# Kernel optimization log

Hardware: AMD Instinct MI355X
Metric: run time of the kernel (lower is better)

Reference implementation:

```python
import jax, jax.numpy as jnp
import numpy as np


def setup_inputs() -> dict:
    key = jax.random.key(0)
    k1, k2, k3 = jax.random.split(key, 3)
    B, F, D = 8192, 4096, 1024
    x = jax.random.normal(k1, (B, D), dtype=jnp.float32)
    mu = jax.random.normal(k2, (F, D), dtype=jnp.float32)
    # keep scales strictly positive and well-conditioned
    scale_diag = jax.random.uniform(k3, (F, D), dtype=jnp.float32, minval=0.5, maxval=1.5)
    return {"x": x, "mu": mu, "scale_diag": scale_diag}


def reference(x, mu, scale_diag):
    # Unnormalized diag-Gaussian log prob for every (batch, feature) pair:
    #   out[b, f] = sum_d -0.5 * ((x[b,d] - mu[f,d]) / scale[f,d])^2
    # Expanded to GEMM form (quadratic expansion):
    #   -0.5 * ( x^2 @ inv2.T  -  2 * x @ (mu*inv2).T  +  sum_d mu^2*inv2 )
    inv2 = 1.0 / (scale_diag * scale_diag)            # [F, D]
    xx = jnp.matmul(x * x, inv2.T)                    # [B, F]
    xm = jnp.matmul(x, (mu * inv2).T)                 # [B, F]
    mm = jnp.sum(mu * mu * inv2, axis=-1)             # [F]
    return -0.5 * (xx - 2.0 * xm + mm[None, :])       # [B, F]
```

## Files before the change

kernel.cpp:

```cpp
#include <hip/hip_runtime.h>
#include <hip/hip_bf16.h>
#include <cstdint>

#define B_SZ 8192
#define F_SZ 4096
#define D_SZ 1024
#define K_SZ 2048

typedef __bf16 bf16x8 __attribute__((ext_vector_type(8)));
typedef float f32x4 __attribute__((ext_vector_type(4)));
typedef float fvec4 __attribute__((ext_vector_type(4)));
typedef unsigned short u16x4 __attribute__((ext_vector_type(4)));

__device__ __forceinline__ unsigned short f2bf(float f) {
    union { float f; unsigned u; } c; c.f = f;
    unsigned r = c.u + 0x7fff + ((c.u >> 16) & 1);
    return (unsigned short)(r >> 16);
}

__device__ __forceinline__ void async16(const void* g, void* l) {
    __builtin_amdgcn_global_load_lds(
        (__attribute__((address_space(1))) void*)g,
        (__attribute__((address_space(3))) void*)l, 16, 0, 0);
}

__global__ __launch_bounds__(256) void prep(const float* __restrict__ x,
                                            const float* __restrict__ mu,
                                            const float* __restrict__ sd,
                                            unsigned short* __restrict__ A,
                                            unsigned short* __restrict__ W,
                                            float* __restrict__ nmm) {
    const int tid = threadIdx.x;
    const int d = tid * 4;
    if (blockIdx.x < B_SZ) {
        const int b = blockIdx.x;
        fvec4 v = __builtin_nontemporal_load(
            (const fvec4*)(x + (size_t)b * D_SZ + d));
        u16x4 xx, xs;
        xx.x = f2bf(v.x * v.x); xx.y = f2bf(v.y * v.y);
        xx.z = f2bf(v.z * v.z); xx.w = f2bf(v.w * v.w);
        xs.x = f2bf(v.x); xs.y = f2bf(v.y); xs.z = f2bf(v.z); xs.w = f2bf(v.w);
        size_t base = (size_t)b * K_SZ;
        *(u16x4*)(A + base + d) = xx;
        *(u16x4*)(A + base + 1024 + d) = xs;
    } else {
        const int f = blockIdx.x - B_SZ;
        size_t off = (size_t)f * D_SZ + d;
        fvec4 m = __builtin_nontemporal_load((const fvec4*)(mu + off));
        fvec4 s = __builtin_nontemporal_load((const fvec4*)(sd + off));
        float i0 = 1.0f / (s.x * s.x), i1 = 1.0f / (s.y * s.y);
        float i2 = 1.0f / (s.z * s.z), i3 = 1.0f / (s.w * s.w);
        u16x4 wi, wm;
        wi.x = f2bf(i0); wi.y = f2bf(i1); wi.z = f2bf(i2); wi.w = f2bf(i3);
        wm.x = f2bf(-2.0f * m.x * i0); wm.y = f2bf(-2.0f * m.y * i1);
        wm.z = f2bf(-2.0f * m.z * i2); wm.w = f2bf(-2.0f * m.w * i3);
        size_t wb = (size_t)f * K_SZ + d;
        *(u16x4*)(W + wb) = wi;
        *(u16x4*)(W + wb + 1024) = wm;
        float mm = m.x * m.x * i0 + m.y * m.y * i1 + m.z * m.z * i2 + m.w * m.w * i3;
        #pragma unroll
        for (int o = 32; o > 0; o >>= 1) mm += __shfl_down(mm, o, 64);
        __shared__ float red[4];
        if ((tid & 63) == 0) red[tid >> 6] = mm;
        __syncthreads();
        if (tid == 0) nmm[f] = -0.5f * (red[0] + red[1] + red[2] + red[3]);
    }
}

__global__ __launch_bounds__(256) void gemm_bt(const unsigned short* __restrict__ A,
                                               const unsigned short* __restrict__ W,
                                               const float* __restrict__ nmm,
                                               float* __restrict__ out) {
    __shared__ __align__(16) unsigned short sA[128 * 32];
    __shared__ __align__(16) unsigned short sB[128 * 32];

    const int tid  = threadIdx.x;
    const int wave = tid >> 6;
    const int lane = tid & 63;
    const int wm = (wave >> 1) * 64;
    const int wn = (wave & 1) * 64;

    const int bid = blockIdx.x;
    const int xcd = bid & 7;
    const int g   = bid >> 3;
    const int tileN = (g & 31) * 128;
    const int tileM = (xcd * 8 + (g >> 5)) * 128;

    const int r16  = lane & 15;
    const int quad = lane >> 4;

    const int row0 = tid >> 2;
    const int col0 = (tid & 3) * 8;
    unsigned short* ldsA0 = sA + (wave * 64) * 8;
    unsigned short* ldsA1 = sA + (256 + wave * 64) * 8;
    unsigned short* ldsB0 = sB + (wave * 64) * 8;
    unsigned short* ldsB1 = sB + (256 + wave * 64) * 8;

    const f32x4 vzero = {0.f, 0.f, 0.f, 0.f};
    f32x4 acc[4][4];
    #pragma unroll
    for (int i = 0; i < 4; ++i)
        #pragma unroll
        for (int j = 0; j < 4; ++j) acc[i][j] = vzero;

    for (int k0 = 0; k0 < K_SZ; k0 += 32) {
        async16(A + (size_t)(tileM + row0) * K_SZ + k0 + col0, ldsA0);
        async16(A + (size_t)(tileM + row0 + 64) * K_SZ + k0 + col0, ldsA1);
        async16(W + (size_t)(tileN + row0) * K_SZ + k0 + col0, ldsB0);
        async16(W + (size_t)(tileN + row0 + 64) * K_SZ + k0 + col0, ldsB1);
        __syncthreads();

        bf16x8 af[4], bfr[4];
        #pragma unroll
        for (int i = 0; i < 4; ++i)
            af[i] = *(const bf16x8*)(sA + (wm + i * 16 + r16) * 32 + quad * 8);
        #pragma unroll
        for (int j = 0; j < 4; ++j)
            bfr[j] = *(const bf16x8*)(sB + (wn + j * 16 + r16) * 32 + quad * 8);
        #pragma unroll
        for (int i = 0; i < 4; ++i)
            #pragma unroll
            for (int j = 0; j < 4; ++j)
                acc[i][j] = __builtin_amdgcn_mfma_f32_16x16x32_bf16(
                    af[i], bfr[j], acc[i][j], 0, 0, 0);
        __syncthreads();
    }

    int   fc[4];
    float cj[4];
    #pragma unroll
    for (int j = 0; j < 4; ++j) {
        fc[j] = tileN + wn + j * 16 + r16;
        cj[j] = nmm[fc[j]];
    }
    #pragma unroll
    for (int i = 0; i < 4; ++i) {
        int mbase = tileM + wm + i * 16 + quad * 4;
        #pragma unroll
        for (int r = 0; r < 4; ++r) {
            float* orow = out + (size_t)(mbase + r) * F_SZ;
            #pragma unroll
            for (int j = 0; j < 4; ++j)
                __builtin_nontemporal_store(-0.5f * acc[i][j][r] + cj[j],
                                            orow + fc[j]);
        }
    }
}

extern "C" void kernel_launch(void* const* d_in, const int* in_sizes, int n_in,
                              void* d_out, int out_size, void* d_ws, size_t ws_size,
                              hipStream_t stream) {
    const float* x  = (const float*)d_in[0];
    const float* mu = (const float*)d_in[1];
    const float* sd = (const float*)d_in[2];
    float* out = (float*)d_out;

    unsigned short* A = (unsigned short*)d_ws;
    unsigned short* W = A + (size_t)B_SZ * K_SZ;
    float* nmm = (float*)(W + (size_t)F_SZ * K_SZ);

    prep<<<B_SZ + F_SZ, 256, 0, stream>>>(x, mu, sd, A, W, nmm);
    gemm_bt<<<(B_SZ / 128) * (F_SZ / 128), 256, 0, stream>>>(A, W, nmm, out);
}
```

Measured before the change: 331.7 us.

## Halve prep blocks, drop XCD tile swizzle and nontemporal memory hints

The prep kernel now has each x-block convert two rows, halving its block count. Loads and stores of inputs and output drop their nontemporal hints. The GEMM replaces its XCD-aware tile remapping with a plain 2D grid, which changes how tiles spread across chiplets and how well the L2 cache is reused. Several unrelated tweaks are bundled together, and the loss of the swizzle could hurt cache locality.

```diff
diff --git a/kernel.cpp b/kernel.cpp
--- a/kernel.cpp
+++ b/kernel.cpp
@@ -31,23 +31,30 @@
                                             unsigned short* __restrict__ W,
                                             float* __restrict__ nmm) {
     const int tid = threadIdx.x;
-    const int d = tid * 4;
-    if (blockIdx.x < B_SZ) {
-        const int b = blockIdx.x;
-        fvec4 v = __builtin_nontemporal_load(
-            (const fvec4*)(x + (size_t)b * D_SZ + d));
-        u16x4 xx, xs;
-        xx.x = f2bf(v.x * v.x); xx.y = f2bf(v.y * v.y);
-        xx.z = f2bf(v.z * v.z); xx.w = f2bf(v.w * v.w);
-        xs.x = f2bf(v.x); xs.y = f2bf(v.y); xs.z = f2bf(v.z); xs.w = f2bf(v.w);
-        size_t base = (size_t)b * K_SZ;
-        *(u16x4*)(A + base + d) = xx;
-        *(u16x4*)(A + base + 1024 + d) = xs;
+    if (blockIdx.x < 4096) {
+        const size_t o0 = (size_t)blockIdx.x * 2048 + tid * 4;
+        fvec4 v0 = *(const fvec4*)(x + o0);
+        fvec4 v1 = *(const fvec4*)(x + o0 + 1024);
+        #pragma unroll
+        for (int h = 0; h < 2; ++h) {
+            fvec4 v = h ? v1 : v0;
+            size_t oo = o0 + h * 1024;
+            size_t b = oo >> 10;
+            int d = (int)(oo & 1023);
+            u16x4 xx, xs;
+            xx.x = f2bf(v.x * v.x); xx.y = f2bf(v.y * v.y);
+            xx.z = f2bf(v.z * v.z); xx.w = f2bf(v.w * v.w);
+            xs.x = f2bf(v.x); xs.y = f2bf(v.y);
+            xs.z = f2bf(v.z); xs.w = f2bf(v.w);
+            *(u16x4*)(A + b * K_SZ + d) = xx;
+            *(u16x4*)(A + b * K_SZ + 1024 + d) = xs;
+        }
     } else {
-        const int f = blockIdx.x - B_SZ;
+        const int f = blockIdx.x - 4096;
+        const int d = tid * 4;
         size_t off = (size_t)f * D_SZ + d;
-        fvec4 m = __builtin_nontemporal_load((const fvec4*)(mu + off));
-        fvec4 s = __builtin_nontemporal_load((const fvec4*)(sd + off));
+        fvec4 m = *(const fvec4*)(mu + off);
+        fvec4 s = *(const fvec4*)(sd + off);
         float i0 = 1.0f / (s.x * s.x), i1 = 1.0f / (s.y * s.y);
         float i2 = 1.0f / (s.z * s.z), i3 = 1.0f / (s.w * s.w);
         u16x4 wi, wm;
@@ -79,13 +86,8 @@
     const int lane = tid & 63;
     const int wm = (wave >> 1) * 64;
     const int wn = (wave & 1) * 64;
-
-    const int bid = blockIdx.x;
-    const int xcd = bid & 7;
-    const int g   = bid >> 3;
-    const int tileN = (g & 31) * 128;
-    const int tileM = (xcd * 8 + (g >> 5)) * 128;
-
+    const int tileM = blockIdx.y * 128;
+    const int tileN = blockIdx.x * 128;
     const int r16  = lane & 15;
     const int quad = lane >> 4;
 
@@ -141,8 +143,7 @@
             float* orow = out + (size_t)(mbase + r) * F_SZ;
             #pragma unroll
             for (int j = 0; j < 4; ++j)
-                __builtin_nontemporal_store(-0.5f * acc[i][j][r] + cj[j],
-                                            orow + fc[j]);
+                orow[fc[j]] = -0.5f * acc[i][j][r] + cj[j];
         }
     }
 }
@@ -159,6 +160,6 @@
     unsigned short* W = A + (size_t)B_SZ * K_SZ;
     float* nmm = (float*)(W + (size_t)F_SZ * K_SZ);
 
-    prep<<<B_SZ + F_SZ, 256, 0, stream>>>(x, mu, sd, A, W, nmm);
-    gemm_bt<<<(B_SZ / 128) * (F_SZ / 128), 256, 0, stream>>>(A, W, nmm, out);
+    prep<<<8192, 256, 0, stream>>>(x, mu, sd, A, W, nmm);
+    gemm_bt<<<dim3(F_SZ / 128, B_SZ / 128), 256, 0, stream>>>(A, W, nmm, out);
 }
```

After: 325.8 us. Within noise of the previous version (-1.8%).
